# Kernel optimization log

Measured on AMD Instinct MI355X. Metric: run time of the kernel, lower is better.

The kernel has to match this reference:

```python
import jax, jax.numpy as jnp
import numpy as np

N_NODES = 100000
N_EDGES = 1600000
IN_DIM = 500
HID = 32
N_REL = 7
OUT_DIM = 4
N_GRAPHS = 16


def setup_inputs() -> dict:
    key = jax.random.key(0)
    ks = jax.random.split(key, 9)
    node_x = jax.random.normal(ks[0], (N_NODES, IN_DIM), dtype=jnp.float32)
    edge_index = jax.random.randint(ks[1], (2, N_EDGES), 0, N_NODES, dtype=jnp.int64)
    edge_attr = jax.random.randint(ks[2], (N_EDGES,), 0, N_REL, dtype=jnp.int64)
    batch = jnp.sort(jax.random.randint(ks[3], (N_NODES,), 0, N_GRAPHS, dtype=jnp.int64))
    # learned params (RGCNConv: per-relation weight, root weight, bias; then fc)
    s_in = 1.0 / np.sqrt(IN_DIM)
    W_rel = jax.random.uniform(ks[4], (N_REL, IN_DIM, HID), jnp.float32, -s_in, s_in)
    W_root = jax.random.uniform(ks[5], (IN_DIM, HID), jnp.float32, -s_in, s_in)
    bias = jnp.zeros((HID,), jnp.float32)
    s_h = 1.0 / np.sqrt(HID)
    fc_w = jax.random.uniform(ks[6], (HID, OUT_DIM), jnp.float32, -s_h, s_h)
    fc_b = jax.random.uniform(ks[7], (OUT_DIM,), jnp.float32, -s_h, s_h)
    return {"node_x": node_x, "edge_index": edge_index, "edge_attr": edge_attr,
            "batch": batch, "W_rel": W_rel, "W_root": W_root, "bias": bias,
            "fc_w": fc_w, "fc_b": fc_b}


def _rgcn(node_x, edge_index, edge_attr, W_rel, W_root, bias):
    # PyG RGCNConv with default aggr='mean': per-relation mean over incoming
    # edges, summed across relations, plus root transform and bias.
    src, dst = edge_index[0], edge_index[1]
    out = node_x @ W_root + bias  # [N, HID]
    for r in range(N_REL):
        h = node_x @ W_rel[r]                       # [N, HID] transform first (cheap: HID << IN_DIM)
        m = (edge_attr == r).astype(node_x.dtype)   # [E] relation mask
        msg = h[src] * m[:, None]                   # [E, HID]
        s = jax.ops.segment_sum(msg, dst, num_segments=N_NODES)
        cnt = jax.ops.segment_sum(m, dst, num_segments=N_NODES)
        out = out + s / jnp.maximum(cnt, 1.0)[:, None]
    return out


def reference(node_x, edge_index, edge_attr, batch, W_rel, W_root, bias, fc_w, fc_b):
    x = _rgcn(node_x, edge_index, edge_attr, W_rel, W_root, bias)
    x = jax.nn.relu(x)
    # global_add_pool over per-node graph ids
    pooled = jax.ops.segment_sum(x, batch, num_segments=N_GRAPHS)  # [B, HID]
    return pooled @ fc_w + fc_b  # [B, OUT_DIM]
```

## Files before the change

kernel.cpp:

```cpp
#include <hip/hip_runtime.h>

#define N_NODES 100000
#define N_EDGES 1600000
#define IN_DIM 500
#define HID 32
#define N_REL 7
#define OUT_DIM 4
#define N_GRAPHS 16
#define NC 256
#define MC 224
#define KPAD 512

#define BK_SHIFT 6
#define BK_NODES 64
#define N_BUCKETS ((N_NODES + BK_NODES - 1) / BK_NODES)
#define NSUB 8
#define SUB_CAP 256
#define BK_CAP (NSUB * SUB_CAP)
#define NPOOL 8

#define GEMM_BLOCKS ((N_NODES + 63) / 64)
#define BIN_BLOCKS  ((N_EDGES + 255) / 256)
#define N_GROUPS 978
#define GRID_MERGED (N_GROUPS * 8)

typedef __attribute__((ext_vector_type(8))) short bf16x8;
typedef __attribute__((ext_vector_type(4))) float f32x4;

__device__ inline unsigned short f2bf(float f) {
    unsigned u = __float_as_uint(f);
    unsigned r = (u + 0x7FFFu + ((u >> 16) & 1u)) >> 16;
    return (unsigned short)r;
}
__device__ inline float bf2f(unsigned short b) {
    return __uint_as_float((unsigned)b << 16);
}

__global__ void build_wbf(const float* __restrict__ W_root,
                          const float* __restrict__ W_rel,
                          unsigned short* __restrict__ Wbf,
                          int* __restrict__ bcur,
                          float* __restrict__ pooled) {
    int idx = blockIdx.x * blockDim.x + threadIdx.x;
    if (idx < N_BUCKETS * NSUB) bcur[idx] = idx * SUB_CAP;
    if (idx < NPOOL * N_GRAPHS * HID) pooled[idx] = 0.f;
    if (idx >= KPAD * NC) return;
    int kk = idx >> 8;
    int n = idx & 255;
    float v = 0.f;
    if (kk < IN_DIM) {
        if (n < HID) v = W_root[kk * HID + n];
        else {
            int r = (n >> 5) - 1;
            v = W_rel[((size_t)r * IN_DIM + kk) * HID + (n & 31)];
        }
    }
    int ks = kk >> 5, q = (kk >> 3) & 3, j = kk & 7;
    Wbf[(size_t)((((ks << 2) + q) << 8) + n) * 8 + j] = f2bf(v);
}

__global__ __launch_bounds__(256, 4) void gemm_bin(const float* __restrict__ A,
                                                   const uint4* __restrict__ Wbf,
                                                   float* __restrict__ Hr,
                                                   unsigned short* __restrict__ Hm,
                                                   const int* __restrict__ src,
                                                   const int* __restrict__ dst,
                                                   const int* __restrict__ attr,
                                                   int* __restrict__ bcur,
                                                   int* __restrict__ rec) {
    const int grp = blockIdx.x >> 3, j8 = blockIdx.x & 7;

    if (grp % 5 != 0) {
        int bb = (grp - grp / 5 - 1) * 8 + j8;
        if (bb >= BIN_BLOCKS) return;
        int e = bb * 256 + threadIdx.x;
        if (e >= N_EDGES) return;
        int d = dst[e];
        int cur = (d >> BK_SHIFT) * NSUB + j8;
        int p = atomicAdd(&bcur[cur], 1);
        if (p < (cur + 1) * SUB_CAP)
            rec[p] = ((d & (BK_NODES - 1)) << 20) | (src[e] << 3) | attr[e];
        return;
    }

    int bid = (grp / 5) * 8 + j8;
    if (bid >= GEMM_BLOCKS) return;

    __shared__ uint4 Alds[32 * 64];

    const int tid = threadIdx.x;
    const int wave = tid >> 6, lane = tid & 63;
    const int l16 = lane & 15, q = lane >> 4;
    const int row0 = bid * 64;
    const int wn = wave * 64;

    int rows_valid = N_NODES - row0; if (rows_valid > 64) rows_valid = 64;
    const float4* Ablk4 = (const float4*)(A + (size_t)row0 * IN_DIM);

    f32x4 acc[4][4];
    #pragma unroll
    for (int mt = 0; mt < 4; mt++)
        #pragma unroll
        for (int nt = 0; nt < 4; nt++)
            #pragma unroll
            for (int r = 0; r < 4; r++) acc[mt][nt][r] = 0.f;

    for (int half = 0; half < 2; half++) {
        if (half) __syncthreads();
        #pragma unroll 4
        for (int it = 0; it < 16; it++) {
            int idx = it * 256 + tid;
            int row = idx >> 6, slot = idx & 63;
            int k = half * 256 + slot * 4;
            float4 v = make_float4(0.f, 0.f, 0.f, 0.f);
            if (row < rows_valid && k < IN_DIM)
                v = Ablk4[row * 125 + (k >> 2)];
            int ksq = slot >> 1;
            int e = (ksq << 6) | ((row ^ ksq) & 63);
            ushort4 b;
            b.x = f2bf(v.x); b.y = f2bf(v.y); b.z = f2bf(v.z); b.w = f2bf(v.w);
            *(ushort4*)((unsigned short*)&Alds[e] + (slot & 1) * 4) = b;
        }
        __syncthreads();
        #pragma unroll 2
        for (int ksl = 0; ksl < 8; ksl++) {
            int ksq_l = ksl * 4 + q;
            int ksq_g = half * 32 + ksq_l;
            bf16x8 bfr[4], afr[4];
            #pragma unroll
            for (int nt = 0; nt < 4; nt++) {
                uint4 t = Wbf[(size_t)(ksq_g << 8) + wn + nt * 16 + l16];
                bfr[nt] = *(bf16x8*)&t;
            }
            #pragma unroll
            for (int mt = 0; mt < 4; mt++)
                afr[mt] = *(const bf16x8*)&Alds[(ksq_l << 6) | (((mt * 16 + l16) ^ ksq_l) & 63)];
            #pragma unroll
            for (int mt = 0; mt < 4; mt++)
                #pragma unroll
                for (int nt = 0; nt < 4; nt++)
                    acc[mt][nt] = __builtin_amdgcn_mfma_f32_16x16x32_bf16(
                        afr[mt], bfr[nt], acc[mt][nt], 0, 0, 0);
        }
    }

    #pragma unroll
    for (int mt = 0; mt < 4; mt++) {
        int rbase = row0 + mt * 16 + q * 4;
        #pragma unroll
        for (int r = 0; r < 4; r++) {
            int row = rbase + r;
            if (row < N_NODES) {
                #pragma unroll
                for (int nt = 0; nt < 4; nt++) {
                    int col = wn + nt * 16 + l16;
                    float v = acc[mt][nt][r];
                    if (wave == 0 && nt < 2)
                        Hr[(size_t)row * HID + col] = v;
                    else
                        Hm[(size_t)row * MC + (col - HID)] = f2bf(v);
                }
            }
        }
    }
}

__global__ __launch_bounds__(256) void bucket_sort(int* __restrict__ rec,
                                                   const int* __restrict__ bcur,
                                                   int* __restrict__ deg,
                                                   int* __restrict__ offs,
                                                   float* __restrict__ invcnt) {
    __shared__ int h2[BK_NODES * N_REL];
    __shared__ int lcur[BK_NODES];
    __shared__ int sorted[BK_CAP];
    __shared__ int scnt[NSUB];
    __shared__ int s_total;

    const int b = blockIdx.x, t = threadIdx.x;
    const int n0 = b << BK_SHIFT;
    const size_t rbase = (size_t)b * BK_CAP;

    for (int i = t; i < BK_NODES * N_REL; i += 256) h2[i] = 0;
    if (t < NSUB) {
        int c = bcur[b * NSUB + t] - (b * NSUB + t) * SUB_CAP;
        scnt[t] = c < SUB_CAP ? c : SUB_CAP;
    }
    __syncthreads();

    for (int s = 0; s < NSUB; s++) {
        int cs = scnt[s];
        const int* rp = rec + rbase + s * SUB_CAP;
        for (int i = t; i < cs; i += 256) {
            int q = rp[i];
            atomicAdd(&h2[(q >> 20) * N_REL + (q & 7)], 1);
        }
    }
    __syncthreads();

    if (t < BK_NODES) {
        int tot = 0;
        #pragma unroll
        for (int r = 0; r < N_REL; r++) tot += h2[t * N_REL + r];
        int incl = tot;
        #pragma unroll
        for (int off = 1; off < BK_NODES; off <<= 1) {
            int y = __shfl_up(incl, off, 64);
            if (t >= off) incl += y;
        }
        int excl = incl - tot;
        lcur[t] = excl;
        if (t == BK_NODES - 1) s_total = incl;
        int n = n0 + t;
        if (n < N_NODES) {
            deg[n] = tot;
            offs[n] = (int)rbase + excl;
        }
    }
    int lim = (N_NODES - n0) * N_REL;
    if (lim > BK_NODES * N_REL) lim = BK_NODES * N_REL;
    for (int i = t; i < lim; i += 256) {
        int cc = h2[i];
        invcnt[(size_t)n0 * N_REL + i] = 1.0f / (float)(cc > 1 ? cc : 1);
    }
    __syncthreads();

    for (int s = 0; s < NSUB; s++) {
        int cs = scnt[s];
        const int* rp = rec + rbase + s * SUB_CAP;
        for (int i = t; i < cs; i += 256) {
            int q = rp[i];
            int p = atomicAdd(&lcur[q >> 20], 1);
            if (p < BK_CAP)
                sorted[p] = q & 0xFFFFF;
        }
    }
    __syncthreads();

    int total = s_total;
    if (total > BK_CAP) total = BK_CAP;
    for (int i = t; i < total; i += 256) rec[rbase + i] = sorted[i];
}

__global__ __launch_bounds__(256) void gather_agg(const int* __restrict__ rec,
                                                  const int* __restrict__ offs,
                                                  const int* __restrict__ deg,
                                                  const float* __restrict__ invcnt,
                                                  const float* __restrict__ bias,
                                                  const unsigned short* __restrict__ Hm,
                                                  const float* __restrict__ Hr,
                                                  const int* __restrict__ batch,
                                                  float* __restrict__ pooled) {
    __shared__ float lpool[N_GRAPHS][HID];
    const int t = threadIdx.x;
    for (int i = t; i < N_GRAPHS * HID; i += 256) ((float*)lpool)[i] = 0.f;
    __syncthreads();

    const int d = blockIdx.x * 8 + (t >> 5);
    const int c = t & 31;

    int dg = deg[d];
    int start = offs[d];
    int end = start + dg;

    float acc = 0.f;
    for (int i = start; i < end; i += 8) {
        int q[8];
        float h[8], w[8];
        #pragma unroll
        for (int j = 0; j < 8; j++) {
            bool ok = (i + j) < end;
            int qq = rec[i + j];
            q[j] = ok ? qq : 0;
            w[j] = ok ? 1.f : 0.f;
        }
        #pragma unroll
        for (int j = 0; j < 8; j++)
            h[j] = bf2f(Hm[(size_t)((q[j] >> 3) & 0x1FFFF) * MC + (q[j] & 7) * HID + c]);
        #pragma unroll
        for (int j = 0; j < 8; j++)
            acc = fmaf(h[j], w[j] * invcnt[d * N_REL + (q[j] & 7)], acc);
    }

    float v = Hr[(size_t)d * HID + c] + bias[c] + acc;
    v = fmaxf(v, 0.f);
    atomicAdd(&lpool[batch[d]][c], v);
    __syncthreads();

    float* pp = pooled + (size_t)(blockIdx.x & (NPOOL - 1)) * N_GRAPHS * HID;
    for (int i2 = t; i2 < N_GRAPHS * HID; i2 += 256) {
        float v2 = ((float*)lpool)[i2];
        if (v2 != 0.f) atomicAdd(&pp[i2], v2);
    }
}

__global__ void fc_kernel(const float* __restrict__ pooled, const float* __restrict__ fc_w,
                          const float* __restrict__ fc_b, float* __restrict__ out) {
    int t = threadIdx.x;
    if (t >= N_GRAPHS * OUT_DIM) return;
    int g = t >> 2, o = t & 3;
    float acc = fc_b[o];
    #pragma unroll
    for (int c = 0; c < HID; c++) {
        float p = 0.f;
        #pragma unroll
        for (int k = 0; k < NPOOL; k++)
            p += pooled[(size_t)(k * N_GRAPHS + g) * HID + c];
        acc += p * fc_w[c * OUT_DIM + o];
    }
    out[t] = acc;
}

extern "C" void kernel_launch(void* const* d_in, const int* in_sizes, int n_in,
                              void* d_out, int out_size, void* d_ws, size_t ws_size,
                              hipStream_t stream) {
    const float* node_x  = (const float*)d_in[0];
    const int*   edge_ix = (const int*)d_in[1];
    const int*   e_attr  = (const int*)d_in[2];
    const int*   batch   = (const int*)d_in[3];
    const float* W_rel   = (const float*)d_in[4];
    const float* W_root  = (const float*)d_in[5];
    const float* bias    = (const float*)d_in[6];
    const float* fc_w    = (const float*)d_in[7];
    const float* fc_b    = (const float*)d_in[8];
    float* out = (float*)d_out;

    char* ws = (char*)d_ws;
    size_t off = 0;
    auto alloc = [&](size_t bytes) {
        char* p = ws + off;
        off += (bytes + 255) & ~(size_t)255;
        return p;
    };
    unsigned short* Wbf = (unsigned short*)alloc((size_t)KPAD * NC * 2);
    float* Hr      = (float*)alloc((size_t)N_NODES * HID * 4);
    unsigned short* Hm = (unsigned short*)alloc((size_t)N_NODES * MC * 2);
    int*   rec     = (int*)  alloc((size_t)N_BUCKETS * BK_CAP * 4);
    int*   bcur    = (int*)  alloc((size_t)N_BUCKETS * NSUB * 4);
    int*   deg     = (int*)  alloc((size_t)N_NODES * 4);
    int*   offsb   = (int*)  alloc((size_t)N_NODES * 4);
    float* invcnt  = (float*)alloc((size_t)N_NODES * N_REL * 4);
    float* pooled  = (float*)alloc((size_t)NPOOL * N_GRAPHS * HID * 4);
    (void)ws_size; (void)in_sizes; (void)n_in; (void)out_size;

    const int* src = edge_ix;
    const int* dst = edge_ix + N_EDGES;

    build_wbf<<<(KPAD * NC + 255) / 256, 256, 0, stream>>>(W_root, W_rel, Wbf,
                                                           bcur, pooled);

    gemm_bin<<<GRID_MERGED, 256, 0, stream>>>(node_x, (const uint4*)Wbf, Hr, Hm,
                                              src, dst, e_attr, bcur, rec);

    bucket_sort<<<N_BUCKETS, 256, 0, stream>>>(rec, bcur, deg, offsb, invcnt);

    gather_agg<<<(N_NODES + 7) / 8, 256, 0, stream>>>(rec, offsb, deg, invcnt,
                                                      bias, Hm, Hr, batch, pooled);

    fc_kernel<<<1, 64, 0, stream>>>(pooled, fc_w, fc_b, out);
}
```

Before: 425.8 us.

## Index bucket sub-slots by hardware XCC ID and prefetch B fragments in GEMM

Edge binning and the pooled partial sums now pick their sub-slot from the hardware XCC ID instead of the block index, so atomics from one chiplet stay on addresses local to that chiplet's L2. SUB_CAP is raised to absorb the less even distribution across sub-slots. The GEMM inner loop now software-pipelines the weight-fragment global loads one k-step ahead and fully unrolls, with launch bounds lowered to 3 waves-per-EU to leave room for the extra registers. The risks are lower occupancy and overflow of a sub-bucket if one XCC's share of edges into a bucket exceeds its capacity.

```diff
diff --git a/kernel.cpp b/kernel.cpp
--- a/kernel.cpp
+++ b/kernel.cpp
@@ -15,7 +15,7 @@
 #define BK_NODES 64
 #define N_BUCKETS ((N_NODES + BK_NODES - 1) / BK_NODES)
 #define NSUB 8
-#define SUB_CAP 256
+#define SUB_CAP 320
 #define BK_CAP (NSUB * SUB_CAP)
 #define NPOOL 8
 
@@ -34,6 +34,11 @@
 }
 __device__ inline float bf2f(unsigned short b) {
     return __uint_as_float((unsigned)b << 16);
+}
+__device__ inline unsigned xcc_id() {
+    unsigned x;
+    asm volatile("s_getreg_b32 %0, hwreg(HW_REG_XCC_ID)" : "=s"(x));
+    return x & 7u;
 }
 
 __global__ void build_wbf(const float* __restrict__ W_root,
@@ -59,7 +64,7 @@
     Wbf[(size_t)((((ks << 2) + q) << 8) + n) * 8 + j] = f2bf(v);
 }
 
-__global__ __launch_bounds__(256, 4) void gemm_bin(const float* __restrict__ A,
+__global__ __launch_bounds__(256, 3) void gemm_bin(const float* __restrict__ A,
                                                    const uint4* __restrict__ Wbf,
                                                    float* __restrict__ Hr,
                                                    unsigned short* __restrict__ Hm,
@@ -75,8 +80,9 @@
         if (bb >= BIN_BLOCKS) return;
         int e = bb * 256 + threadIdx.x;
         if (e >= N_EDGES) return;
+        unsigned xcc = xcc_id();
         int d = dst[e];
-        int cur = (d >> BK_SHIFT) * NSUB + j8;
+        int cur = (d >> BK_SHIFT) * NSUB + (int)xcc;
         int p = atomicAdd(&bcur[cur], 1);
         if (p < (cur + 1) * SUB_CAP)
             rec[p] = ((d & (BK_NODES - 1)) << 20) | (src[e] << 3) | attr[e];
@@ -122,16 +128,30 @@
             *(ushort4*)((unsigned short*)&Alds[e] + (slot & 1) * 4) = b;
         }
         __syncthreads();
-        #pragma unroll 2
+        bf16x8 bnxt[4];
+        {
+            int kg0 = (half * 32 + q) << 8;
+            #pragma unroll
+            for (int nt = 0; nt < 4; nt++) {
+                uint4 t = Wbf[(size_t)kg0 + wn + nt * 16 + l16];
+                bnxt[nt] = *(bf16x8*)&t;
+            }
+        }
+        #pragma unroll
         for (int ksl = 0; ksl < 8; ksl++) {
+            bf16x8 bcur4[4];
+            #pragma unroll
+            for (int nt = 0; nt < 4; nt++) bcur4[nt] = bnxt[nt];
+            if (ksl < 7) {
+                int kg = (half * 32 + (ksl + 1) * 4 + q) << 8;
+                #pragma unroll
+                for (int nt = 0; nt < 4; nt++) {
+                    uint4 t = Wbf[(size_t)kg + wn + nt * 16 + l16];
+                    bnxt[nt] = *(bf16x8*)&t;
+                }
+            }
             int ksq_l = ksl * 4 + q;
-            int ksq_g = half * 32 + ksq_l;
-            bf16x8 bfr[4], afr[4];
-            #pragma unroll
-            for (int nt = 0; nt < 4; nt++) {
-                uint4 t = Wbf[(size_t)(ksq_g << 8) + wn + nt * 16 + l16];
-                bfr[nt] = *(bf16x8*)&t;
-            }
+            bf16x8 afr[4];
             #pragma unroll
             for (int mt = 0; mt < 4; mt++)
                 afr[mt] = *(const bf16x8*)&Alds[(ksq_l << 6) | (((mt * 16 + l16) ^ ksq_l) & 63)];
@@ -140,7 +160,7 @@
                 #pragma unroll
                 for (int nt = 0; nt < 4; nt++)
                     acc[mt][nt] = __builtin_amdgcn_mfma_f32_16x16x32_bf16(
-                        afr[mt], bfr[nt], acc[mt][nt], 0, 0, 0);
+                        afr[mt], bcur4[nt], acc[mt][nt], 0, 0, 0);
         }
     }
 
@@ -286,7 +306,7 @@
     atomicAdd(&lpool[batch[d]][c], v);
     __syncthreads();
 
-    float* pp = pooled + (size_t)(blockIdx.x & (NPOOL - 1)) * N_GRAPHS * HID;
+    float* pp = pooled + (size_t)xcc_id() * N_GRAPHS * HID;
     for (int i2 = t; i2 < N_GRAPHS * HID; i2 += 256) {
         float v2 = ((float*)lpool)[i2];
         if (v2 != 0.f) atomicAdd(&pp[i2], v2);
```

After: 438.6 us. 3.0% more time.
